# Kernel optimization log

Hardware: AMD Instinct MI355X
Metric: run time of the kernel (lower is better)

Reference implementation:

```python
import jax, jax.numpy as jnp
import numpy as np

N, E, F, ED, H, C, B = 50000, 200000, 768, 768, 256, 3, 4096


def setup_inputs() -> dict:
    key = jax.random.key(0)
    ks = jax.random.split(key, 20)
    s = 0.05  # init scale for params
    inp = {
        "x": jax.random.normal(ks[0], (N, F), jnp.float32),
        "edge_attr": jax.random.normal(ks[1], (E, ED), jnp.float32),
        # GATConv layer 1 (in=F, out=H, heads=1, edge_dim=ED)
        "W1": jax.random.normal(ks[2], (F, H), jnp.float32) * s,
        "as1": jax.random.normal(ks[3], (H,), jnp.float32) * s,
        "ad1": jax.random.normal(ks[4], (H,), jnp.float32) * s,
        "We1": jax.random.normal(ks[5], (ED, H), jnp.float32) * s,
        "ae1": jax.random.normal(ks[6], (H,), jnp.float32) * s,
        "b1": jnp.zeros((H,), jnp.float32),
        # GATConv layer 2 (in=H, out=H)
        "W2": jax.random.normal(ks[7], (H, H), jnp.float32) * s,
        "as2": jax.random.normal(ks[8], (H,), jnp.float32) * s,
        "ad2": jax.random.normal(ks[9], (H,), jnp.float32) * s,
        "We2": jax.random.normal(ks[10], (ED, H), jnp.float32) * s,
        "ae2": jax.random.normal(ks[11], (H,), jnp.float32) * s,
        "b2": jnp.zeros((H,), jnp.float32),
        # prediction head
        "Wp": jax.random.normal(ks[12], (H, C), jnp.float32) * s,
        "bp": jnp.zeros((C,), jnp.float32),
        "edge_index": jax.random.randint(ks[13], (2, E), 0, N, jnp.int32),
        "nodes": jax.random.randint(ks[14], (2, B), 0, N, jnp.int32),
    }
    return inp


def gat_conv(x, edge_attr, src, dst, W, a_src, a_dst, We, a_e, b, n):
    # GATConv, heads=1, edge_dim attention, add_self_loops=False
    xl = x @ W  # [n, H]
    alpha_src = (xl * a_src).sum(-1)  # [n]
    alpha_dst = (xl * a_dst).sum(-1)  # [n]
    alpha_edge = ((edge_attr @ We) * a_e).sum(-1)  # [E]
    alpha = alpha_src[src] + alpha_dst[dst] + alpha_edge  # [E]
    alpha = jax.nn.leaky_relu(alpha, 0.2)
    # scatter-softmax over incoming edges of each destination node
    m = jax.ops.segment_max(alpha, dst, num_segments=n)
    e = jnp.exp(alpha - m[dst])
    den = jax.ops.segment_sum(e, dst, num_segments=n)
    coef = e / den[dst]  # [E]
    out = jax.ops.segment_sum(coef[:, None] * xl[src], dst, num_segments=n)
    return out + b


def reference(x, edge_attr, W1, as1, ad1, We1, ae1, b1, W2, as2, ad2, We2, ae2, b2, Wp, bp, edge_index, nodes):
    src, dst = edge_index[0], edge_index[1]
    n = x.shape[0]
    h = jax.nn.relu(gat_conv(x, edge_attr, src, dst, W1, as1, ad1, We1, ae1, b1, n))
    titles = gat_conv(h, edge_attr, src, dst, W2, as2, ad2, We2, ae2, b2, n)
    c = titles[nodes[0]] * titles[nodes[1]]  # [B, H]
    return c @ Wp + bp
```

## Files before the change

### kernel.cpp

```cpp
#include <hip/hip_runtime.h>
#include <math.h>

#define HDIM 256
#define FDIM 768
#define BM 128
#define BK 32

typedef __attribute__((ext_vector_type(8))) short short8;
typedef __attribute__((ext_vector_type(4))) float f32x4;
typedef __attribute__((ext_vector_type(4))) unsigned short us4;

__device__ __forceinline__ unsigned short f2bf(float f) {
  unsigned int u = __float_as_uint(f);
  unsigned int r = (u + 0x7FFFu + ((u >> 16) & 1u)) >> 16;
  return (unsigned short)r;
}
__device__ __forceinline__ float bf2f(unsigned short b) {
  return __uint_as_float(((unsigned int)b) << 16);
}

__device__ __forceinline__ void gload_lds16(const void* g, void* l) {
  __builtin_amdgcn_global_load_lds(
      (const __attribute__((address_space(1))) void*)g,
      (__attribute__((address_space(3))) void*)l, 16, 0, 0);
}


__global__ void k_scan1(const int* __restrict__ cnt, int* __restrict__ offsets,
                        int* __restrict__ bsums, int n) {
  __shared__ int s[256];
  int i = blockIdx.x * 256 + threadIdx.x;
  int v = (i < n) ? cnt[i] : 0;
  s[threadIdx.x] = v;
  __syncthreads();
  for (int off = 1; off < 256; off <<= 1) {
    int t = (threadIdx.x >= off) ? s[threadIdx.x - off] : 0;
    __syncthreads();
    s[threadIdx.x] += t;
    __syncthreads();
  }
  if (i < n) offsets[i + 1] = s[threadIdx.x];
  if (threadIdx.x == 255) bsums[blockIdx.x] = s[255];
}

__global__ void k_scan23(int* __restrict__ offsets, int* __restrict__ cursor,
                         const int* __restrict__ bsums, int n) {
  __shared__ int s2[256];
  __shared__ int sBase;
  const int nb = (n + 255) / 256;
  const int t = threadIdx.x;
  const int bid = blockIdx.x;
  int vv = (t < nb) ? bsums[t] : 0;
  s2[t] = vv;
  __syncthreads();
  for (int off = 1; off < 256; off <<= 1) {
    int tv = (t >= off) ? s2[t - off] : 0;
    __syncthreads();
    s2[t] += tv;
    __syncthreads();
  }
  if (t == 0) sBase = (bid > 0) ? s2[bid - 1] : 0;
  __syncthreads();
  int base = sBase;
  int i = bid * 256 + t;
  if (i < n) {
    int v = offsets[i + 1] + base;
    offsets[i + 1] = v;
    if (i + 1 < n) cursor[i + 1] = v;
    if (i == 0) { offsets[0] = 0; cursor[0] = 0; }
  }
}

__global__ void k_scatter(const int* __restrict__ dst, int* __restrict__ cursor,
                          int* __restrict__ elist, int E) {
  int e = blockIdx.x * 256 + threadIdx.x;
  if (e < E) {
    int p = atomicAdd(&cursor[dst[e]], 1);
    elist[p] = e;
  }
}


__global__ __launch_bounds__(256) void k_prep(
    const float* __restrict__ We1, const float* __restrict__ ae1,
    const float* __restrict__ We2, const float* __restrict__ ae2,
    float* __restrict__ v1, float* __restrict__ v2,
    const float* __restrict__ W1, unsigned short* __restrict__ W1t,
    const float* __restrict__ W2, unsigned short* __restrict__ W2t,
    const int* __restrict__ dstArr, int* __restrict__ cnt, int E) {
  int bid = blockIdx.x;
  if (bid < 384) {
    int row = bid * 4 + (threadIdx.x >> 6);
    int lane = threadIdx.x & 63;
    const float* W = (row < FDIM) ? We1 : We2;
    const float* a = (row < FDIM) ? ae1 : ae2;
    int r = (row < FDIM) ? row : row - FDIM;
    float4 w = *(const float4*)&W[(size_t)r * HDIM + lane * 4];
    float4 av = *(const float4*)&a[lane * 4];
    float p = w.x * av.x + w.y * av.y + w.z * av.z + w.w * av.w;
    #pragma unroll
    for (int off = 32; off; off >>= 1) p += __shfl_down(p, off, 64);
    if (lane == 0) ((row < FDIM) ? v1 : v2)[r] = p;
  } else if (bid < 640) {
    int nn = bid - 384;
    for (int k = threadIdx.x; k < FDIM; k += 256)
      W1t[(size_t)nn * FDIM + k] = f2bf(W1[(size_t)k * HDIM + nn]);
  } else if (bid < 896) {
    int nn = bid - 640;
    for (int k = threadIdx.x; k < HDIM; k += 256)
      W2t[(size_t)nn * HDIM + k] = f2bf(W2[(size_t)k * HDIM + nn]);
  } else {
    int e = (bid - 896) * 256 + threadIdx.x;
    if (e < E) atomicAdd(&cnt[dstArr[e]], 1);
  }
}


template <bool AF32, bool COUTBF>
__device__ __forceinline__ void gemm_body(unsigned char* lds,
                                          const void* __restrict__ Ain,
                                          const unsigned short* __restrict__ Bt,
                                          void* __restrict__ Cout,
                                          float* __restrict__ sOut,
                                          float* __restrict__ dOut,
                                          const float* __restrict__ a_src,
                                          const float* __restrict__ a_dst,
                                          int M, int K, int tile) {
  unsigned char* As = lds;
  unsigned char* Bs = lds + 8192;
  float* partS = (float*)(lds + 24576);
  float* partD = (float*)(lds + 24576 + 2048);
  const int t = threadIdx.x;
  const int l = t & 63;
  const int w = t >> 6;
  const int wm = w >> 2, wn = w & 3;
  const int bm = tile * BM;

  f32x4 acc[4][4] = {};

  int rowA = bm + (t & 127);
  if (rowA >= M) rowA = M - 1;
  const int cA = t >> 7;
  int rowAr = bm + (t >> 2);
  if (rowAr >= M) rowAr = M - 1;
  const int kbAr = t & 3;
  const int sAr = kbAr * 2048 + (t >> 2) * 16;
  const int nB = t & 255;
  const int cB0 = t >> 8;
  const int cB1 = 2 + (t >> 8);

  int aAddr[4], bAddr[4];
  #pragma unroll
  for (int mt = 0; mt < 4; ++mt) {
    int m = wm * 64 + mt * 16 + (l & 15);
    aAddr[mt] = (l >> 4) * 2048 + m * 16;
  }
  #pragma unroll
  for (int nt = 0; nt < 4; ++nt) {
    int nn = wn * 64 + nt * 16 + (l & 15);
    bAddr[nt] = (l >> 4) * 4096 + nn * 16;
  }

  const int nsteps = K / BK;
  for (int ks = 0; ks < nsteps; ++ks) {
    const int k0 = ks * BK;
    __syncthreads();
    if (AF32) {
      const float* A = (const float*)Ain;
      const float* p = A + (size_t)rowAr * K + k0 + kbAr * 8;
      float4 f0 = *(const float4*)p;
      float4 f1 = *(const float4*)(p + 4);
      short8 hv;
      hv[0] = (short)f2bf(f0.x); hv[1] = (short)f2bf(f0.y);
      hv[2] = (short)f2bf(f0.z); hv[3] = (short)f2bf(f0.w);
      hv[4] = (short)f2bf(f1.x); hv[5] = (short)f2bf(f1.y);
      hv[6] = (short)f2bf(f1.z); hv[7] = (short)f2bf(f1.w);
      *(short8*)(As + sAr) = hv;
    } else {
      const unsigned short* A = (const unsigned short*)Ain;
      gload_lds16(A + (size_t)rowA * K + k0 + cA * 8, As + t * 16);
    }
    gload_lds16(Bt + (size_t)nB * K + k0 + cB0 * 8, Bs + t * 16);
    gload_lds16(Bt + (size_t)nB * K + k0 + cB1 * 8, Bs + 8192 + t * 16);
    __syncthreads();

    short8 af[4], bfr[4];
    #pragma unroll
    for (int mt = 0; mt < 4; ++mt) af[mt] = *(const short8*)(As + aAddr[mt]);
    #pragma unroll
    for (int nt = 0; nt < 4; ++nt) bfr[nt] = *(const short8*)(Bs + bAddr[nt]);
    #pragma unroll
    for (int mt = 0; mt < 4; ++mt)
      #pragma unroll
      for (int nt = 0; nt < 4; ++nt)
        acc[mt][nt] = __builtin_amdgcn_mfma_f32_16x16x32_bf16(af[mt], bfr[nt], acc[mt][nt], 0, 0, 0);
  }

  float asv[4], adv[4];
  #pragma unroll
  for (int nt = 0; nt < 4; ++nt) {
    int col = wn * 64 + nt * 16 + (l & 15);
    asv[nt] = a_src[col];
    adv[nt] = a_dst[col];
  }
  #pragma unroll
  for (int mt = 0; mt < 4; ++mt) {
    int rloc = wm * 64 + mt * 16 + ((l >> 4) << 2);
    #pragma unroll
    for (int r = 0; r < 4; ++r) {
      int row = bm + rloc + r;
      float ps = 0.f, pd = 0.f;
      #pragma unroll
      for (int nt = 0; nt < 4; ++nt) {
        float v = acc[mt][nt][r];
        if (row < M) {
          int col = wn * 64 + nt * 16 + (l & 15);
          if (COUTBF)
            ((unsigned short*)Cout)[(size_t)row * HDIM + col] = f2bf(v);
          else
            ((float*)Cout)[(size_t)row * HDIM + col] = v;
        }
        ps += v * asv[nt];
        pd += v * adv[nt];
      }
      #pragma unroll
      for (int off = 1; off < 16; off <<= 1) {
        ps += __shfl_xor(ps, off, 64);
        pd += __shfl_xor(pd, off, 64);
      }
      if ((l & 15) == 0) {
        partS[wn * 128 + rloc + r] = ps;
        partD[wn * 128 + rloc + r] = pd;
      }
    }
  }
  __syncthreads();
  if (t < 128) {
    int row = bm + t;
    if (row < M) {
      sOut[row] = partS[t] + partS[128 + t] + partS[256 + t] + partS[384 + t];
      dOut[row] = partD[t] + partD[128 + t] + partD[256 + t] + partD[384 + t];
    }
  }
}


__device__ __forceinline__ void edge_body(unsigned char* lds,
                                          const float* __restrict__ ea,
                                          const float* __restrict__ v1,
                                          const float* __restrict__ v2,
                                          float* __restrict__ o1,
                                          float* __restrict__ o2, int E, int ebid) {
  float* sv1 = (float*)lds;
  float* sv2 = (float*)(lds + 3072);
  for (int i = threadIdx.x; i < FDIM; i += 512) { sv1[i] = v1[i]; sv2[i] = v2[i]; }
  __syncthreads();
  int e = ebid * 8 + (threadIdx.x >> 6);
  if (e >= E) return;
  int lane = threadIdx.x & 63;
  const float* row = ea + (size_t)e * FDIM;
  float p1 = 0.f, p2 = 0.f;
  #pragma unroll
  for (int t = 0; t < 3; ++t) {
    int idx = t * 256 + lane * 4;
    float4 x = *(const float4*)&row[idx];
    float4 a = *(const float4*)&sv1[idx];
    float4 b = *(const float4*)&sv2[idx];
    p1 += x.x * a.x + x.y * a.y + x.z * a.z + x.w * a.w;
    p2 += x.x * b.x + x.y * b.y + x.z * b.z + x.w * b.w;
  }
  #pragma unroll
  for (int off = 32; off; off >>= 1) {
    p1 += __shfl_down(p1, off, 64);
    p2 += __shfl_down(p2, off, 64);
  }
  if (lane == 0) { o1[e] = p1; o2[e] = p2; }
}


__global__ __launch_bounds__(512) void k_fat1(
    const float* __restrict__ x, const unsigned short* __restrict__ W1t,
    unsigned short* __restrict__ xl1b, float* __restrict__ sArr, float* __restrict__ dArr,
    const float* __restrict__ as1, const float* __restrict__ ad1, int M,
    const float* __restrict__ ea, const float* __restrict__ v1,
    const float* __restrict__ v2, float* __restrict__ ae1Arr,
    float* __restrict__ ae2Arr, int E, int nGemm) {
  __shared__ unsigned char lds[28672];
  if ((int)blockIdx.x < nGemm)
    gemm_body<true, true>(lds, x, W1t, xl1b, sArr, dArr, as1, ad1, M, FDIM, blockIdx.x);
  else
    edge_body(lds, ea, v1, v2, ae1Arr, ae2Arr, E, blockIdx.x - nGemm);
}

__global__ __launch_bounds__(512) void k_gemm2(
    const unsigned short* __restrict__ hb, const unsigned short* __restrict__ W2t,
    unsigned short* __restrict__ xl2b, float* __restrict__ sArr, float* __restrict__ dArr,
    const float* __restrict__ as2, const float* __restrict__ ad2, int M) {
  __shared__ unsigned char lds[28672];
  gemm_body<false, true>(lds, hb, W2t, xl2b, sArr, dArr, as2, ad2, M, HDIM, blockIdx.x);
}


__device__ __forceinline__ void agg_node(const unsigned short* __restrict__ xlb,
                                         const float* __restrict__ sArr,
                                         float dnode,
                                         const float* __restrict__ aeArr,
                                         const int* __restrict__ src,
                                         const int* __restrict__ elist,
                                         int beg, int end, int lane,
                                         float& a0, float& a1, float& a2, float& a3) {
  float run_m = -1e30f, run_den = 0.f;
  a0 = a1 = a2 = a3 = 0.f;
  for (int c0 = beg; c0 < end; c0 += 64) {
    int j = c0 + lane;
    float al = -1e30f;
    int sj = 0;
    if (j < end) {
      int e = elist[j];
      sj = src[e];
      float a = sArr[sj] + dnode + aeArr[e];
      al = (a > 0.f) ? a : 0.2f * a;
    }
    float cm = al;
    #pragma unroll
    for (int off = 32; off; off >>= 1) cm = fmaxf(cm, __shfl_xor(cm, off, 64));
    float new_m = fmaxf(run_m, cm);
    float ev = (j < end) ? expf(al - new_m) : 0.f;
    float csum = ev;
    #pragma unroll
    for (int off = 32; off; off >>= 1) csum += __shfl_xor(csum, off, 64);
    float scale = expf(run_m - new_m);
    run_den = run_den * scale + csum;
    a0 *= scale; a1 *= scale; a2 *= scale; a3 *= scale;
    int cdeg = end - c0;
    if (cdeg > 64) cdeg = 64;
    for (int q = 0; q < cdeg; ++q) {
      float wgt = __shfl(ev, q, 64);
      int sq = __shfl(sj, q, 64);
      us4 v = *(const us4*)(xlb + (size_t)sq * HDIM + lane * 4);
      a0 += wgt * bf2f(v[0]); a1 += wgt * bf2f(v[1]);
      a2 += wgt * bf2f(v[2]); a3 += wgt * bf2f(v[3]);
    }
    run_m = new_m;
  }
  float inv = (end > beg) ? 1.f / run_den : 0.f;
  a0 *= inv; a1 *= inv; a2 *= inv; a3 *= inv;
}


__global__ __launch_bounds__(256) void k_aggregate1(const unsigned short* __restrict__ xlb,
                                                    const float* __restrict__ sArr,
                                                    const float* __restrict__ dArr,
                                                    const float* __restrict__ aeArr,
                                                    const int* __restrict__ src,
                                                    const int* __restrict__ offsets,
                                                    const int* __restrict__ elist,
                                                    const float* __restrict__ bias,
                                                    unsigned short* __restrict__ outb,
                                                    int n) {
  int node = blockIdx.x * 4 + (threadIdx.x >> 6);
  if (node >= n) return;
  int lane = threadIdx.x & 63;
  int beg = offsets[node], end = offsets[node + 1];
  float a0, a1, a2, a3;
  agg_node(xlb, sArr, dArr[node], aeArr, src, elist, beg, end, lane, a0, a1, a2, a3);
  float4 bv = *(const float4*)(bias + lane * 4);
  float o0 = fmaxf(a0 + bv.x, 0.f), o1 = fmaxf(a1 + bv.y, 0.f);
  float o2 = fmaxf(a2 + bv.z, 0.f), o3 = fmaxf(a3 + bv.w, 0.f);
  us4 ov;
  ov[0] = f2bf(o0); ov[1] = f2bf(o1); ov[2] = f2bf(o2); ov[3] = f2bf(o3);
  *(us4*)(outb + (size_t)node * HDIM + lane * 4) = ov;
}


__global__ __launch_bounds__(256) void k_agg2head(const unsigned short* __restrict__ xl2b,
                                                  const float* __restrict__ sArr,
                                                  const float* __restrict__ dArr,
                                                  const float* __restrict__ aeArr,
                                                  const int* __restrict__ src,
                                                  const int* __restrict__ offsets,
                                                  const int* __restrict__ elist,
                                                  const float* __restrict__ b2,
                                                  const int* __restrict__ nodes,
                                                  const float* __restrict__ Wp,
                                                  const float* __restrict__ bp,
                                                  float* __restrict__ out, int Bn) {
  __shared__ float tls[2][2][HDIM];
  int wv = threadIdx.x >> 6;
  int lane = threadIdx.x & 63;
  int pl = wv >> 1;
  int side = wv & 1;
  int b = blockIdx.x * 2 + pl;
  if (b < Bn) {
    int node = nodes[side * Bn + b];
    int beg = offsets[node], end = offsets[node + 1];
    float a0, a1, a2, a3;
    agg_node(xl2b, sArr, dArr[node], aeArr, src, elist, beg, end, lane, a0, a1, a2, a3);
    float4 bv = *(const float4*)(b2 + lane * 4);
    float* dstp = &tls[pl][side][lane * 4];
    dstp[0] = a0 + bv.x; dstp[1] = a1 + bv.y;
    dstp[2] = a2 + bv.z; dstp[3] = a3 + bv.w;
  }
  __syncthreads();
  if (b < Bn && side == 0) {
    float4 t0 = *(const float4*)&tls[pl][0][lane * 4];
    float4 t1 = *(const float4*)&tls[pl][1][lane * 4];
    float c0 = t0.x * t1.x, c1 = t0.y * t1.y, c2 = t0.z * t1.z, c3 = t0.w * t1.w;
    int h0 = lane * 4;
    float s0 = c0 * Wp[h0 * 3 + 0] + c1 * Wp[(h0 + 1) * 3 + 0] +
               c2 * Wp[(h0 + 2) * 3 + 0] + c3 * Wp[(h0 + 3) * 3 + 0];
    float s1 = c0 * Wp[h0 * 3 + 1] + c1 * Wp[(h0 + 1) * 3 + 1] +
               c2 * Wp[(h0 + 2) * 3 + 1] + c3 * Wp[(h0 + 3) * 3 + 1];
    float s2 = c0 * Wp[h0 * 3 + 2] + c1 * Wp[(h0 + 1) * 3 + 2] +
               c2 * Wp[(h0 + 2) * 3 + 2] + c3 * Wp[(h0 + 3) * 3 + 2];
    #pragma unroll
    for (int off = 32; off; off >>= 1) {
      s0 += __shfl_down(s0, off, 64);
      s1 += __shfl_down(s1, off, 64);
      s2 += __shfl_down(s2, off, 64);
    }
    if (lane == 0) {
      out[b * 3 + 0] = s0 + bp[0];
      out[b * 3 + 1] = s1 + bp[1];
      out[b * 3 + 2] = s2 + bp[2];
    }
  }
}


extern "C" void kernel_launch(void* const* d_in, const int* in_sizes, int n_in,
                              void* d_out, int out_size, void* d_ws, size_t ws_size,
                              hipStream_t stream) {
  const float* x         = (const float*)d_in[0];
  const float* edge_attr = (const float*)d_in[1];
  const float* W1  = (const float*)d_in[2];
  const float* as1 = (const float*)d_in[3];
  const float* ad1 = (const float*)d_in[4];
  const float* We1 = (const float*)d_in[5];
  const float* ae1 = (const float*)d_in[6];
  const float* b1  = (const float*)d_in[7];
  const float* W2  = (const float*)d_in[8];
  const float* as2 = (const float*)d_in[9];
  const float* ad2 = (const float*)d_in[10];
  const float* We2 = (const float*)d_in[11];
  const float* ae2 = (const float*)d_in[12];
  const float* b2  = (const float*)d_in[13];
  const float* Wp  = (const float*)d_in[14];
  const float* bp  = (const float*)d_in[15];
  const int* edge_index = (const int*)d_in[16];
  const int* nodes      = (const int*)d_in[17];

  const int N  = in_sizes[0] / FDIM;
  const int E  = in_sizes[16] / 2;
  const int Bn = in_sizes[17] / 2;
  const int* srcArr = edge_index;
  const int* dstArr = edge_index + E;

  char* w = (char*)d_ws;
  auto carve = [&](size_t bytes) -> void* {
    void* p = (void*)w;
    w += (bytes + 255) & ~(size_t)255;
    return p;
  };
  unsigned short* xl1b   = (unsigned short*)carve(2 * (size_t)N * HDIM);
  unsigned short* hb     = (unsigned short*)carve(2 * (size_t)N * HDIM);
  unsigned short* W1t    = (unsigned short*)carve(2 * (size_t)FDIM * HDIM);
  unsigned short* W2t    = (unsigned short*)carve(2 * (size_t)HDIM * HDIM);
  float* ae1Arr = (float*)carve(sizeof(float) * E);
  float* ae2Arr = (float*)carve(sizeof(float) * E);
  float* sArr = (float*)carve(sizeof(float) * N);
  float* dArr = (float*)carve(sizeof(float) * N);
  float* v1 = (float*)carve(sizeof(float) * FDIM);
  float* v2 = (float*)carve(sizeof(float) * FDIM);
  int* cnt     = (int*)carve(sizeof(int) * N);
  int* offsets = (int*)carve(sizeof(int) * (N + 1));
  int* cursor  = (int*)carve(sizeof(int) * N);
  int* elist   = (int*)carve(sizeof(int) * E);
  int* bsums   = (int*)carve(sizeof(int) * 256);

  const int nbScan = (N + 255) / 256;
  const int nbHist = (E + 255) / 256;
  const int nGemm = (N + BM - 1) / BM;
  const int nEdge = (E + 7) / 8;

  hipMemsetAsync(cnt, 0, sizeof(int) * N, stream);
  k_prep<<<896 + nbHist, 256, 0, stream>>>(We1, ae1, We2, ae2, v1, v2,
                                           W1, W1t, W2, W2t, dstArr, cnt, E);
  k_scan1<<<nbScan, 256, 0, stream>>>(cnt, offsets, bsums, N);
  k_scan23<<<nbScan, 256, 0, stream>>>(offsets, cursor, bsums, N);
  k_scatter<<<nbHist, 256, 0, stream>>>(dstArr, cursor, elist, E);

  k_fat1<<<nGemm + nEdge, 512, 0, stream>>>(x, W1t, xl1b, sArr, dArr, as1, ad1, N,
                                            edge_attr, v1, v2, ae1Arr, ae2Arr, E, nGemm);
  k_aggregate1<<<(N + 3) / 4, 256, 0, stream>>>(xl1b, sArr, dArr, ae1Arr, srcArr,
                                                offsets, elist, b1, hb, N);
  k_gemm2<<<nGemm, 512, 0, stream>>>(hb, W2t, xl1b, sArr, dArr, as2, ad2, N);
  k_agg2head<<<(Bn + 1) / 2, 256, 0, stream>>>(xl1b, sArr, dArr, ae2Arr, srcArr,
                                               offsets, elist, b2, nodes, Wp, bp,
                                               (float*)d_out, Bn);
}
```

Before: 289.9 us.

## Merge two-pass scan into single-pass decoupled scan and fold scatter into fat kernel

Replaces the two scan kernels with one single-pass scan. Each block publishes its sum behind a release flag, and later blocks spin on the earlier flags to build their prefix. The edge-list scatter kernel is removed, and its work now runs in 98 extra blocks inside the fused GEMM/edge kernel. This cuts two kernel launches and their serialization gaps. In exchange it relies on the spin-wait never deadlocking, since earlier blocks must be resident, and the flags are cleared in the existing memset.

```diff
diff --git a/kernel.cpp b/kernel.cpp
--- a/kernel.cpp
+++ b/kernel.cpp
@@ -23,61 +23,6 @@
   __builtin_amdgcn_global_load_lds(
       (const __attribute__((address_space(1))) void*)g,
       (__attribute__((address_space(3))) void*)l, 16, 0, 0);
-}
-
-
-__global__ void k_scan1(const int* __restrict__ cnt, int* __restrict__ offsets,
-                        int* __restrict__ bsums, int n) {
-  __shared__ int s[256];
-  int i = blockIdx.x * 256 + threadIdx.x;
-  int v = (i < n) ? cnt[i] : 0;
-  s[threadIdx.x] = v;
-  __syncthreads();
-  for (int off = 1; off < 256; off <<= 1) {
-    int t = (threadIdx.x >= off) ? s[threadIdx.x - off] : 0;
-    __syncthreads();
-    s[threadIdx.x] += t;
-    __syncthreads();
-  }
-  if (i < n) offsets[i + 1] = s[threadIdx.x];
-  if (threadIdx.x == 255) bsums[blockIdx.x] = s[255];
-}
-
-__global__ void k_scan23(int* __restrict__ offsets, int* __restrict__ cursor,
-                         const int* __restrict__ bsums, int n) {
-  __shared__ int s2[256];
-  __shared__ int sBase;
-  const int nb = (n + 255) / 256;
-  const int t = threadIdx.x;
-  const int bid = blockIdx.x;
-  int vv = (t < nb) ? bsums[t] : 0;
-  s2[t] = vv;
-  __syncthreads();
-  for (int off = 1; off < 256; off <<= 1) {
-    int tv = (t >= off) ? s2[t - off] : 0;
-    __syncthreads();
-    s2[t] += tv;
-    __syncthreads();
-  }
-  if (t == 0) sBase = (bid > 0) ? s2[bid - 1] : 0;
-  __syncthreads();
-  int base = sBase;
-  int i = bid * 256 + t;
-  if (i < n) {
-    int v = offsets[i + 1] + base;
-    offsets[i + 1] = v;
-    if (i + 1 < n) cursor[i + 1] = v;
-    if (i == 0) { offsets[0] = 0; cursor[0] = 0; }
-  }
-}
-
-__global__ void k_scatter(const int* __restrict__ dst, int* __restrict__ cursor,
-                          int* __restrict__ elist, int E) {
-  int e = blockIdx.x * 256 + threadIdx.x;
-  if (e < E) {
-    int p = atomicAdd(&cursor[dst[e]], 1);
-    elist[p] = e;
-  }
 }
 
 
@@ -112,6 +57,52 @@
   } else {
     int e = (bid - 896) * 256 + threadIdx.x;
     if (e < E) atomicAdd(&cnt[dstArr[e]], 1);
+  }
+}
+
+
+__global__ __launch_bounds__(256) void k_scan_lb(const int* __restrict__ cnt,
+                                                 int* __restrict__ offsets,
+                                                 int* __restrict__ cursor,
+                                                 int* __restrict__ bsums,
+                                                 int* __restrict__ flags, int n) {
+  __shared__ int s[256];
+  __shared__ int r[256];
+  const int b = blockIdx.x, t = threadIdx.x;
+  int i = b * 256 + t;
+  int v = (i < n) ? cnt[i] : 0;
+  s[t] = v;
+  __syncthreads();
+  for (int off = 1; off < 256; off <<= 1) {
+    int tv = (t >= off) ? s[t - off] : 0;
+    __syncthreads();
+    s[t] += tv;
+    __syncthreads();
+  }
+  if (t == 255) {
+    bsums[b] = s[255];
+    __threadfence();
+    __hip_atomic_store(&flags[b], 1, __ATOMIC_RELEASE, __HIP_MEMORY_SCOPE_AGENT);
+  }
+  int contrib = 0;
+  if (t < b) {
+    while (!__hip_atomic_load(&flags[t], __ATOMIC_ACQUIRE, __HIP_MEMORY_SCOPE_AGENT))
+      __builtin_amdgcn_s_sleep(2);
+    contrib = bsums[t];
+  }
+  r[t] = contrib;
+  __syncthreads();
+  #pragma unroll
+  for (int off = 128; off; off >>= 1) {
+    if (t < off) r[t] += r[t + off];
+    __syncthreads();
+  }
+  int base = r[0];
+  if (i < n) {
+    int incl = base + s[t];
+    offsets[i + 1] = incl;
+    cursor[i] = incl - v;
+    if (i == 0) offsets[0] = 0;
   }
 }
 
@@ -278,18 +269,30 @@
 }
 
 
+#define NSCAT 98
+
 __global__ __launch_bounds__(512) void k_fat1(
     const float* __restrict__ x, const unsigned short* __restrict__ W1t,
     unsigned short* __restrict__ xl1b, float* __restrict__ sArr, float* __restrict__ dArr,
     const float* __restrict__ as1, const float* __restrict__ ad1, int M,
     const float* __restrict__ ea, const float* __restrict__ v1,
     const float* __restrict__ v2, float* __restrict__ ae1Arr,
-    float* __restrict__ ae2Arr, int E, int nGemm) {
+    float* __restrict__ ae2Arr, int E, int nGemm,
+    const int* __restrict__ dstArr, int* __restrict__ cursor,
+    int* __restrict__ elist) {
   __shared__ unsigned char lds[28672];
-  if ((int)blockIdx.x < nGemm)
-    gemm_body<true, true>(lds, x, W1t, xl1b, sArr, dArr, as1, ad1, M, FDIM, blockIdx.x);
-  else
-    edge_body(lds, ea, v1, v2, ae1Arr, ae2Arr, E, blockIdx.x - nGemm);
+  int bid = blockIdx.x;
+  if (bid < nGemm) {
+    gemm_body<true, true>(lds, x, W1t, xl1b, sArr, dArr, as1, ad1, M, FDIM, bid);
+  } else if (bid < nGemm + NSCAT) {
+    int sb = bid - nGemm;
+    for (int e = sb * 512 + threadIdx.x; e < E; e += NSCAT * 512) {
+      int p = atomicAdd(&cursor[dstArr[e]], 1);
+      elist[p] = e;
+    }
+  } else {
+    edge_body(lds, ea, v1, v2, ae1Arr, ae2Arr, E, bid - nGemm - NSCAT);
+  }
 }
 
 __global__ __launch_bounds__(512) void k_gemm2(
@@ -472,26 +475,28 @@
   float* dArr = (float*)carve(sizeof(float) * N);
   float* v1 = (float*)carve(sizeof(float) * FDIM);
   float* v2 = (float*)carve(sizeof(float) * FDIM);
-  int* cnt     = (int*)carve(sizeof(int) * N);
+  int* cntflags = (int*)carve(sizeof(int) * (N + 256));
   int* offsets = (int*)carve(sizeof(int) * (N + 1));
   int* cursor  = (int*)carve(sizeof(int) * N);
   int* elist   = (int*)carve(sizeof(int) * E);
   int* bsums   = (int*)carve(sizeof(int) * 256);
 
+  int* cnt = cntflags;
+  int* flags = cntflags + N;
+
   const int nbScan = (N + 255) / 256;
   const int nbHist = (E + 255) / 256;
   const int nGemm = (N + BM - 1) / BM;
   const int nEdge = (E + 7) / 8;
 
-  hipMemsetAsync(cnt, 0, sizeof(int) * N, stream);
+  hipMemsetAsync(cntflags, 0, sizeof(int) * (N + 256), stream);
   k_prep<<<896 + nbHist, 256, 0, stream>>>(We1, ae1, We2, ae2, v1, v2,
                                            W1, W1t, W2, W2t, dstArr, cnt, E);
-  k_scan1<<<nbScan, 256, 0, stream>>>(cnt, offsets, bsums, N);
-  k_scan23<<<nbScan, 256, 0, stream>>>(offsets, cursor, bsums, N);
-  k_scatter<<<nbHist, 256, 0, stream>>>(dstArr, cursor, elist, E);
-
-  k_fat1<<<nGemm + nEdge, 512, 0, stream>>>(x, W1t, xl1b, sArr, dArr, as1, ad1, N,
-                                            edge_attr, v1, v2, ae1Arr, ae2Arr, E, nGemm);
+  k_scan_lb<<<nbScan, 256, 0, stream>>>(cnt, offsets, cursor, bsums, flags, N);
+
+  k_fat1<<<nGemm + NSCAT + nEdge, 512, 0, stream>>>(
+      x, W1t, xl1b, sArr, dArr, as1, ad1, N,
+      edge_attr, v1, v2, ae1Arr, ae2Arr, E, nGemm, dstArr, cursor, elist);
   k_aggregate1<<<(N + 3) / 4, 256, 0, stream>>>(xl1b, sArr, dArr, ae1Arr, srcArr,
                                                 offsets, elist, b1, hb, N);
   k_gemm2<<<nGemm, 512, 0, stream>>>(hb, W2t, xl1b, sArr, dArr, as2, ad2, N);
```

After: 294.2 us. No clear change (+1.5%).
